# Performance work log

Measured on AMD Instinct MI355X. Metric: run time of the kernel, lower is better.

The kernel has to match this reference:

```python
import jax, jax.numpy as jnp
import numpy as np

B, DA, DU, W, MODES, L = 32, 2, 1, 64, 16, 8192


def setup_inputs() -> dict:
    key = jax.random.key(0)
    ks = jax.random.split(key, 9)
    x = jax.random.normal(ks[0], (B, DA, L), dtype=jnp.float32)
    P_w = jax.random.normal(ks[1], (W, DA), dtype=jnp.float32) * 0.1
    P_b = jax.random.normal(ks[2], (W,), dtype=jnp.float32) * 0.1
    # 4 spectral blocks: complex weights stored as real/imag parts [4, modes, out, in]
    scale = 1.0 / (W * W)
    k_wr = jax.random.uniform(ks[3], (4, MODES, W, W), dtype=jnp.float32) * scale
    k_wi = jax.random.uniform(ks[4], (4, MODES, W, W), dtype=jnp.float32) * scale
    conv_w = jax.random.normal(ks[5], (4, W, W), dtype=jnp.float32) * 0.1
    conv_b = jax.random.normal(ks[6], (4, W), dtype=jnp.float32) * 0.1
    Q_w = jax.random.normal(ks[7], (DU, W), dtype=jnp.float32) * 0.1
    Q_b = jax.random.normal(ks[8], (DU,), dtype=jnp.float32) * 0.1
    return {"x": x, "P_w": P_w, "P_b": P_b, "k_wr": k_wr, "k_wi": k_wi,
            "conv_w": conv_w, "conv_b": conv_b, "Q_w": Q_w, "Q_b": Q_b}


def _spectral(h, wr, wi):
    # h: [B, C, L]; wr/wi: [modes, O, I]
    hf = jnp.fft.rfft(h, axis=-1)                      # [B, C, F] complex
    w = wr + 1j * wi
    out_m = jnp.einsum('koi,bik->bok', w, hf[:, :, :MODES])  # [B, O, modes]
    F = hf.shape[-1]
    pad = jnp.zeros((h.shape[0], w.shape[1], F - MODES), dtype=out_m.dtype)
    full = jnp.concatenate([out_m, pad], axis=-1)
    return jnp.fft.irfft(full, n=h.shape[-1], axis=-1)


def reference(x, P_w, P_b, k_wr, k_wi, conv_w, conv_b, Q_w, Q_b):
    # lifting 1x1 conv: [B, da, L] -> [B, W, L]
    h = jnp.einsum('oc,bcl->bol', P_w, x) + P_b[None, :, None]
    for i in range(4):
        x1 = _spectral(h, k_wr[i], k_wi[i])
        x2 = jnp.einsum('oc,bcl->bol', conv_w[i], h) + conv_b[i][None, :, None]
        h = jax.nn.gelu(x1 + x2, approximate=False)
    out = jnp.einsum('oc,bcl->bol', Q_w, h) + Q_b[None, :, None]
    return out
```

## Files before the change

kernel.cpp:

```cpp
#include <hip/hip_runtime.h>
#include <math.h>

#define B 32
#define DA 2
#define DU 1
#define W 64
#define MODES 16
#define L 8192
#define LMASK 8191
#define LT 128

typedef __attribute__((ext_vector_type(8))) short short8;
typedef __attribute__((ext_vector_type(4))) float floatx4;

#define N_H (B*W*L)
#define OFF_H 0
#define N_HF (B*W*MODES)
#define OFF_HFR (OFF_H + N_H)
#define OFF_HFI (OFF_HFR + N_HF)
#define N_GT (B*W*32)
#define OFF_GT  (OFF_HFI + N_HF)
#define OFF_BTH (OFF_GT + N_GT)
#define N_BTW (32*L/2)
#define OFF_BTL (OFF_BTH + N_BTW)
#define OFF_BFH (OFF_BTL + N_BTW)
#define N_BF (256*2*16*32/2)
#define OFF_BFL (OFF_BFH + N_BF)
#define OFF_CWH (OFF_BFL + N_BF)
#define OFF_CWL (OFF_CWH + 8192)
#define OFF_P2  (OFF_CWL + 8192)

__device__ __forceinline__ unsigned packsplit(float v) {
    unsigned u = __float_as_uint(v);
    unsigned hi = u & 0xffff0000u;
    float lo = v - __uint_as_float(hi);
    return hi | (__float_as_uint(lo) >> 16);
}
__device__ __forceinline__ void fsplit(float v, unsigned short& h, unsigned short& l) {
    unsigned u = __float_as_uint(v);
    h = (unsigned short)(u >> 16);
    float lof = v - __uint_as_float(u & 0xffff0000u);
    l = (unsigned short)(__float_as_uint(lof) >> 16);
}

__global__ void k_tables(short* __restrict__ BTh, short* __restrict__ BTl,
                         short* __restrict__ BFhi, short* __restrict__ BFlo,
                         const float* __restrict__ cw,
                         short* __restrict__ CWFh, short* __restrict__ CWFl) {
    if (blockIdx.x < 512) {
        int idx = blockIdx.x * 256 + threadIdx.x;
        if (idx >= MODES * L) return;
        int k = idx >> 13;
        int l = idx & LMASK;
        int m = (k * l) & LMASK;
        float ang = 6.28318530717958647692f * ((float)m / (float)L);
        float s, c;
        sincosf(ang, &s, &c);
        unsigned short hh, ll;
        fsplit(c, hh, ll);
        BTh[(size_t)l * 32 + k] = (short)hh;  BTl[(size_t)l * 32 + k] = (short)ll;
        int sstep = l >> 5, qj = l & 31;
        int idx_re = ((sstep * 2 + 0) * 16 + k) * 32 + qj;
        BFhi[idx_re] = (short)hh;  BFlo[idx_re] = (short)ll;
        fsplit(s, hh, ll);
        BTh[(size_t)l * 32 + 16 + k] = (short)hh;  BTl[(size_t)l * 32 + 16 + k] = (short)ll;
        unsigned short nh, nl;
        fsplit(-s, nh, nl);
        int idx_im = ((sstep * 2 + 1) * 16 + k) * 32 + qj;
        BFhi[idx_im] = (short)nh;  BFlo[idx_im] = (short)nl;
    } else {
        int idx = (blockIdx.x - 512) * 256 + threadIdx.x;
        if (idx >= 4 * W * W) return;
        int layer = idx >> 12;
        int r = idx & 4095;
        int o = r >> 6, c = r & 63;
        int ot = o >> 4, n = o & 15, Kc = c >> 5, rest = c & 31;
        unsigned short hh, ll;
        fsplit(cw[idx], hh, ll);
        int di = layer * 4096 + ((ot * 2 + Kc) * 16 + n) * 32 + rest;
        CWFh[di] = (short)hh;  CWFl[di] = (short)ll;
    }
}

__device__ __forceinline__ void dft_partial(const unsigned* HsL,
                                            const short* __restrict__ BFhi,
                                            const short* __restrict__ BFlo,
                                            float* __restrict__ part2,
                                            int b, int l0, int t) {
    int wv = t >> 6, lane = t & 63, quad = lane >> 4, n = lane & 15;
    int sbase = l0 >> 5;
    const unsigned* arow = HsL + (wv * 16 + n) * 132 + quad * 8;
    floatx4 accR = {0.f, 0.f, 0.f, 0.f}, accI = {0.f, 0.f, 0.f, 0.f};
#pragma unroll
    for (int ks = 0; ks < 4; ks++) {
        const uint4* ap = (const uint4*)(arow + ks * 32);
        uint4 a0 = ap[0], a1 = ap[1];
        unsigned av[8] = {a0.x, a0.y, a0.z, a0.w, a1.x, a1.y, a1.z, a1.w};
        union { short8 v; unsigned short u[8]; } ah, al;
#pragma unroll
        for (int j = 0; j < 8; j++) {
            ah.u[j] = (unsigned short)(av[j] >> 16);
            al.u[j] = (unsigned short)(av[j] & 0xffffu);
        }
        int s = sbase + ks;
        const short* bb = BFhi + ((size_t)(s * 2) * 16 + n) * 32 + quad * 8;
        const short* lb = BFlo + ((size_t)(s * 2) * 16 + n) * 32 + quad * 8;
        short8 BhR = *(const short8*)bb;
        short8 BlR = *(const short8*)lb;
        short8 BhI = *(const short8*)(bb + 512);
        short8 BlI = *(const short8*)(lb + 512);
        accR = __builtin_amdgcn_mfma_f32_16x16x32_bf16(ah.v, BhR, accR, 0, 0, 0);
        accR = __builtin_amdgcn_mfma_f32_16x16x32_bf16(ah.v, BlR, accR, 0, 0, 0);
        accR = __builtin_amdgcn_mfma_f32_16x16x32_bf16(al.v, BhR, accR, 0, 0, 0);
        accI = __builtin_amdgcn_mfma_f32_16x16x32_bf16(ah.v, BhI, accI, 0, 0, 0);
        accI = __builtin_amdgcn_mfma_f32_16x16x32_bf16(ah.v, BlI, accI, 0, 0, 0);
        accI = __builtin_amdgcn_mfma_f32_16x16x32_bf16(al.v, BhI, accI, 0, 0, 0);
    }
    float* pr = part2 + (size_t)(l0 >> 7) * 65536
                      + ((size_t)b * 64 + wv * 16 + quad * 4) * 32 + n;
#pragma unroll
    for (int r = 0; r < 4; r++) {
        pr[(size_t)r * 32]      = accR[r];
        pr[(size_t)r * 32 + 16] = accI[r];
    }
}

__global__ __launch_bounds__(256) void k_lift(const float* __restrict__ x,
                                              const float* __restrict__ Pw,
                                              const float* __restrict__ Pb,
                                              unsigned* __restrict__ h,
                                              const short* __restrict__ BFhi,
                                              const short* __restrict__ BFlo,
                                              float* __restrict__ part2) {
    __shared__ unsigned HsL[64 * 132];
    int t = threadIdx.x;
    int b = blockIdx.y;
    int l0 = blockIdx.x * LT;
    int lq = t & 31, c8 = t >> 5;
    float4 x0 = *((const float4*)(x + (size_t)(b * 2 + 0) * L + l0) + lq);
    float4 x1 = *((const float4*)(x + (size_t)(b * 2 + 1) * L + l0) + lq);
#pragma unroll
    for (int cc = 0; cc < 8; cc++) {
        int c = c8 * 8 + cc;
        float w0 = Pw[c * 2 + 0], w1 = Pw[c * 2 + 1], pb = Pb[c];
        uint4 pv;
        pv.x = packsplit(fmaf(w0, x0.x, fmaf(w1, x1.x, pb)));
        pv.y = packsplit(fmaf(w0, x0.y, fmaf(w1, x1.y, pb)));
        pv.z = packsplit(fmaf(w0, x0.z, fmaf(w1, x1.z, pb)));
        pv.w = packsplit(fmaf(w0, x0.w, fmaf(w1, x1.w, pb)));
        *(uint4*)(h + ((size_t)b * W + c) * L + l0 + lq * 4) = pv;
        *(uint4*)&HsL[c * 132 + lq * 4] = pv;
    }
    __syncthreads();
    dft_partial(HsL, BFhi, BFlo, part2, b, l0, t);
}

__global__ void k_red(const float* __restrict__ part2, float* __restrict__ hf) {
    int idx = blockIdx.x * 256 + threadIdx.x;
    float s = 0.f;
#pragma unroll 16
    for (int c = 0; c < 64; c++) s += part2[(size_t)c * 65536 + idx];
    int row = idx >> 5, kp = idx & 31;
    if (kp < 16) hf[row * 16 + kp] = s;
    else         hf[32768 + row * 16 + (kp - 16)] = s;
}

__global__ __launch_bounds__(256) void k_mix(const float* __restrict__ hfr,
                                             const float* __restrict__ hfi,
                                             const float* __restrict__ kwr,
                                             const float* __restrict__ kwi,
                                             unsigned* __restrict__ Gt) {
    __shared__ float wrT[64 * 65], wiT[64 * 65];
    int t = threadIdx.x;
    int k = blockIdx.x;
    const float* wr = kwr + k * 4096;
    const float* wi = kwi + k * 4096;
    for (int i = t; i < 4096; i += 256) {
        int o = i >> 6, c = i & 63;
        wrT[c * 65 + o] = wr[i];
        wiT[c * 65 + o] = wi[i];
    }
    __syncthreads();
    int o = t & 63, bq = t >> 6;
    int b = blockIdx.y * 4 + bq;
    float accr = 0.f, acci = 0.f;
#pragma unroll 8
    for (int c = 0; c < W; c++) {
        float hr = hfr[(b * 64 + c) * 16 + k];
        float hi = hfi[(b * 64 + c) * 16 + k];
        float wrv = wrT[c * 65 + o], wiv = wiT[c * 65 + o];
        accr = fmaf(wrv, hr, fmaf(-wiv, hi, accr));
        acci = fmaf(wrv, hi, fmaf(wiv, hr, acci));
    }
    float sc = (k == 0) ? (1.f / (float)L) : (2.f / (float)L);
    float gi = (k == 0) ? 0.f : -acci * sc;
    Gt[((size_t)b * 64 + o) * 32 + k]      = packsplit(accr * sc);
    Gt[((size_t)b * 64 + o) * 32 + 16 + k] = packsplit(gi);
}

__device__ __forceinline__ float erf_fast(float x) {
    float ax = fabsf(x);
    float tinv = __builtin_amdgcn_rcpf(fmaf(0.3275911f, ax, 1.f));
    float p = fmaf(1.061405429f, tinv, -1.453152027f);
    p = fmaf(p, tinv, 1.421413741f);
    p = fmaf(p, tinv, -0.284496736f);
    p = fmaf(p, tinv, 0.254829592f);
    p = p * tinv;
    float e = fmaf(-p, __expf(-ax * ax), 1.f);
    return copysignf(e, x);
}

__global__ __launch_bounds__(256, 4) void k_combine(
    unsigned* __restrict__ h, const short* __restrict__ BTh, const short* __restrict__ BTl,
    const unsigned* __restrict__ Gt,
    const short* __restrict__ cwfh, const short* __restrict__ cwfl,
    const float* __restrict__ cb,
    const short* __restrict__ BFhi, const short* __restrict__ BFlo,
    float* __restrict__ part2, int emit,
    const float* __restrict__ Qw, const float* __restrict__ Qb,
    float* __restrict__ outbuf, int proj) {
    __shared__ unsigned Hs[64 * 132];
    int t = threadIdx.x;
    int b = blockIdx.y;
    int l0 = blockIdx.x * LT;

    int lane = t & 63, wv = t >> 6;
    int quad = lane >> 4, n = lane & 15;

    unsigned rawB[2][2][8];
    short8 Th[2], Tl[2];
#pragma unroll
    for (int lt = 0; lt < 2; lt++) {
        int lg = l0 + wv * 32 + lt * 16 + n;
        const unsigned* hb = h + (size_t)b * W * L + lg;
#pragma unroll
        for (int Kc = 0; Kc < 2; Kc++) {
#pragma unroll
            for (int j = 0; j < 8; j++) {
                int c = Kc * 32 + quad * 8 + j;
                rawB[lt][Kc][j] = hb[(size_t)c * L];
            }
        }
        Th[lt] = *(const short8*)(BTh + (size_t)lg * 32 + quad * 8);
        Tl[lt] = *(const short8*)(BTl + (size_t)lg * 32 + quad * 8);
    }
    short8 Bh[2][2], Bl[2][2];
#pragma unroll
    for (int lt = 0; lt < 2; lt++) {
#pragma unroll
        for (int Kc = 0; Kc < 2; Kc++) {
            union { short8 v; unsigned short u[8]; } uh, ul;
#pragma unroll
            for (int j = 0; j < 8; j++) {
                unsigned x = rawB[lt][Kc][j];
                uh.u[j] = (unsigned short)(x >> 16);
                ul.u[j] = (unsigned short)(x & 0xffffu);
            }
            Bh[lt][Kc] = uh.v; Bl[lt][Kc] = ul.v;
        }
    }

    float pacc[2] = {0.f, 0.f};

#pragma unroll 2
    for (int ot = 0; ot < 4; ot++) {
        int oa = ot * 16 + n;
        short8 Wh[2], Wl[2];
#pragma unroll
        for (int Kc = 0; Kc < 2; Kc++) {
            int wi = ((ot * 2 + Kc) * 16 + n) * 32 + quad * 8;
            Wh[Kc] = *(const short8*)(cwfh + wi);
            Wl[Kc] = *(const short8*)(cwfl + wi);
        }
        short8 Gh, Gl;
        {
            const uint4* gp = (const uint4*)(Gt + ((size_t)b * W + oa) * 32 + quad * 8);
            uint4 g0 = gp[0], g1 = gp[1];
            unsigned gv[8] = {g0.x, g0.y, g0.z, g0.w, g1.x, g1.y, g1.z, g1.w};
            union { short8 v; unsigned short u[8]; } ah, al;
#pragma unroll
            for (int j = 0; j < 8; j++) {
                ah.u[j] = (unsigned short)(gv[j] >> 16);
                al.u[j] = (unsigned short)(gv[j] & 0xffffu);
            }
            Gh = ah.v; Gl = al.v;
        }

#pragma unroll
        for (int lt = 0; lt < 2; lt++) {
            floatx4 acc = {0.f, 0.f, 0.f, 0.f};
#pragma unroll
            for (int Kc = 0; Kc < 2; Kc++) {
                acc = __builtin_amdgcn_mfma_f32_16x16x32_bf16(Wh[Kc], Bh[lt][Kc], acc, 0, 0, 0);
                acc = __builtin_amdgcn_mfma_f32_16x16x32_bf16(Wh[Kc], Bl[lt][Kc], acc, 0, 0, 0);
                acc = __builtin_amdgcn_mfma_f32_16x16x32_bf16(Wl[Kc], Bh[lt][Kc], acc, 0, 0, 0);
            }
            acc = __builtin_amdgcn_mfma_f32_16x16x32_bf16(Gh, Th[lt], acc, 0, 0, 0);
            acc = __builtin_amdgcn_mfma_f32_16x16x32_bf16(Gh, Tl[lt], acc, 0, 0, 0);
            acc = __builtin_amdgcn_mfma_f32_16x16x32_bf16(Gl, Th[lt], acc, 0, 0, 0);
            int lloc = wv * 32 + lt * 16 + n;
            int lg = l0 + lloc;
#pragma unroll
            for (int r = 0; r < 4; r++) {
                int od = ot * 16 + quad * 4 + r;
                float v = acc[r] + cb[od];
                float g = 0.5f * v * (1.f + erf_fast(v * 0.70710678118654752440f));
                if (proj) {
                    pacc[lt] = fmaf(Qw[od], g, pacc[lt]);
                } else {
                    unsigned p = packsplit(g);
                    h[((size_t)b * W + od) * L + lg] = p;
                    if (emit) Hs[od * 132 + lloc] = p;
                }
            }
        }
    }
    if (emit) {
        __syncthreads();
        dft_partial(Hs, BFhi, BFlo, part2, b, l0, t);
    }
    if (proj) {
        float qb = Qb[0];
#pragma unroll
        for (int lt = 0; lt < 2; lt++) {
            float v = pacc[lt];
            v += __shfl_xor(v, 16, 64);
            v += __shfl_xor(v, 32, 64);
            if (quad == 0)
                outbuf[(size_t)b * L + l0 + wv * 32 + lt * 16 + n] = v + qb;
        }
    }
}

extern "C" void kernel_launch(void* const* d_in, const int* in_sizes, int n_in,
                              void* d_out, int out_size, void* d_ws, size_t ws_size,
                              hipStream_t stream) {
    const float* x   = (const float*)d_in[0];
    const float* Pw  = (const float*)d_in[1];
    const float* Pb  = (const float*)d_in[2];
    const float* kwr = (const float*)d_in[3];
    const float* kwi = (const float*)d_in[4];
    const float* cw  = (const float*)d_in[5];
    const float* cb  = (const float*)d_in[6];
    const float* Qw  = (const float*)d_in[7];
    const float* Qb  = (const float*)d_in[8];

    float* ws = (float*)d_ws;
    unsigned* h    = (unsigned*)(ws + OFF_H);
    float*    hfr  = ws + OFF_HFR;
    float*    hfi  = ws + OFF_HFI;
    unsigned* Gt   = (unsigned*)(ws + OFF_GT);
    short*    BTh  = (short*)(ws + OFF_BTH);
    short*    BTl  = (short*)(ws + OFF_BTL);
    short*    BFhi = (short*)(ws + OFF_BFH);
    short*    BFlo = (short*)(ws + OFF_BFL);
    short*    CWFh = (short*)(ws + OFF_CWH);
    short*    CWFl = (short*)(ws + OFF_CWL);
    float*    part2 = ws + OFF_P2;

    k_tables<<<512 + 64, 256, 0, stream>>>(BTh, BTl, BFhi, BFlo, cw, CWFh, CWFl);
    k_lift<<<dim3(L / LT, B), 256, 0, stream>>>(x, Pw, Pb, h, BFhi, BFlo, part2);

    for (int i = 0; i < 4; i++) {
        k_red<<<65536 / 256, 256, 0, stream>>>(part2, hfr);
        k_mix<<<dim3(MODES, B / 4), 256, 0, stream>>>(hfr, hfi,
                                                      kwr + (size_t)i * MODES * W * W,
                                                      kwi + (size_t)i * MODES * W * W,
                                                      Gt);
        k_combine<<<dim3(L / LT, B), 256, 0, stream>>>(h, BTh, BTl, Gt,
                                                       CWFh + (size_t)i * 4096,
                                                       CWFl + (size_t)i * 4096,
                                                       cb + (size_t)i * W,
                                                       BFhi, BFlo, part2,
                                                       (i < 3) ? 1 : 0,
                                                       Qw, Qb, (float*)d_out,
                                                       (i == 3) ? 1 : 0);
    }
}
```

Before: 298.7 us.

## Replace partial-sum buffer and reduction kernel with atomic accumulation into double-buffered spectra

The DFT partials were written to a large per-tile buffer and summed by a separate k_red kernel. They are now accumulated directly into a spectrum buffer with float atomics. Two spectrum buffers alternate, with the next one zeroed inside k_mix and the first zeroed in k_tables. This removes one kernel launch per layer and a large partial-buffer write/read. The shared-memory tile also drops its padding in favour of an XOR swizzle, and launch bounds rise to 5 blocks per CU. The costs are atomic contention on 64K addresses and nondeterministic summation order.

```diff
diff --git a/kernel.cpp b/kernel.cpp
--- a/kernel.cpp
+++ b/kernel.cpp
@@ -16,10 +16,10 @@
 #define N_H (B*W*L)
 #define OFF_H 0
 #define N_HF (B*W*MODES)
-#define OFF_HFR (OFF_H + N_H)
-#define OFF_HFI (OFF_HFR + N_HF)
+#define OFF_HF0 (OFF_H + N_H)
+#define OFF_HF1 (OFF_HF0 + 2*N_HF)
 #define N_GT (B*W*32)
-#define OFF_GT  (OFF_HFI + N_HF)
+#define OFF_GT  (OFF_HF1 + 2*N_HF)
 #define OFF_BTH (OFF_GT + N_GT)
 #define N_BTW (32*L/2)
 #define OFF_BTL (OFF_BTH + N_BTW)
@@ -28,7 +28,6 @@
 #define OFF_BFL (OFF_BFH + N_BF)
 #define OFF_CWH (OFF_BFL + N_BF)
 #define OFF_CWL (OFF_CWH + 8192)
-#define OFF_P2  (OFF_CWL + 8192)
 
 __device__ __forceinline__ unsigned packsplit(float v) {
     unsigned u = __float_as_uint(v);
@@ -46,7 +45,8 @@
 __global__ void k_tables(short* __restrict__ BTh, short* __restrict__ BTl,
                          short* __restrict__ BFhi, short* __restrict__ BFlo,
                          const float* __restrict__ cw,
-                         short* __restrict__ CWFh, short* __restrict__ CWFl) {
+                         short* __restrict__ CWFh, short* __restrict__ CWFl,
+                         float* __restrict__ hf0) {
     if (blockIdx.x < 512) {
         int idx = blockIdx.x * 256 + threadIdx.x;
         if (idx >= MODES * L) return;
@@ -68,7 +68,7 @@
         fsplit(-s, nh, nl);
         int idx_im = ((sstep * 2 + 1) * 16 + k) * 32 + qj;
         BFhi[idx_im] = (short)nh;  BFlo[idx_im] = (short)nl;
-    } else {
+    } else if (blockIdx.x < 576) {
         int idx = (blockIdx.x - 512) * 256 + threadIdx.x;
         if (idx >= 4 * W * W) return;
         int layer = idx >> 12;
@@ -79,22 +79,29 @@
         fsplit(cw[idx], hh, ll);
         int di = layer * 4096 + ((ot * 2 + Kc) * 16 + n) * 32 + rest;
         CWFh[di] = (short)hh;  CWFl[di] = (short)ll;
+    } else {
+        int idx = (blockIdx.x - 576) * 256 + threadIdx.x;
+        float4 z = {0.f, 0.f, 0.f, 0.f};
+        *(float4*)(hf0 + (size_t)idx * 4) = z;
     }
 }
 
 __device__ __forceinline__ void dft_partial(const unsigned* HsL,
                                             const short* __restrict__ BFhi,
                                             const short* __restrict__ BFlo,
-                                            float* __restrict__ part2,
+                                            float* __restrict__ hfacc,
                                             int b, int l0, int t) {
     int wv = t >> 6, lane = t & 63, quad = lane >> 4, n = lane & 15;
     int sbase = l0 >> 5;
-    const unsigned* arow = HsL + (wv * 16 + n) * 132 + quad * 8;
+    int c = wv * 16 + n;
+    int swz = (c & 7) << 2;
+    const unsigned* arow = HsL + c * 128;
     floatx4 accR = {0.f, 0.f, 0.f, 0.f}, accI = {0.f, 0.f, 0.f, 0.f};
 #pragma unroll
     for (int ks = 0; ks < 4; ks++) {
-        const uint4* ap = (const uint4*)(arow + ks * 32);
-        uint4 a0 = ap[0], a1 = ap[1];
+        int col = quad * 8 + ks * 32;
+        uint4 a0 = *(const uint4*)(arow + (col ^ swz));
+        uint4 a1 = *(const uint4*)(arow + ((col + 4) ^ swz));
         unsigned av[8] = {a0.x, a0.y, a0.z, a0.w, a1.x, a1.y, a1.z, a1.w};
         union { short8 v; unsigned short u[8]; } ah, al;
 #pragma unroll
@@ -116,23 +123,22 @@
         accI = __builtin_amdgcn_mfma_f32_16x16x32_bf16(ah.v, BlI, accI, 0, 0, 0);
         accI = __builtin_amdgcn_mfma_f32_16x16x32_bf16(al.v, BhI, accI, 0, 0, 0);
     }
-    float* pr = part2 + (size_t)(l0 >> 7) * 65536
-                      + ((size_t)b * 64 + wv * 16 + quad * 4) * 32 + n;
+    float* pr = hfacc + ((size_t)(b * 64 + wv * 16 + quad * 4)) * 16 + n;
 #pragma unroll
     for (int r = 0; r < 4; r++) {
-        pr[(size_t)r * 32]      = accR[r];
-        pr[(size_t)r * 32 + 16] = accI[r];
-    }
-}
-
-__global__ __launch_bounds__(256) void k_lift(const float* __restrict__ x,
-                                              const float* __restrict__ Pw,
-                                              const float* __restrict__ Pb,
-                                              unsigned* __restrict__ h,
-                                              const short* __restrict__ BFhi,
-                                              const short* __restrict__ BFlo,
-                                              float* __restrict__ part2) {
-    __shared__ unsigned HsL[64 * 132];
+        unsafeAtomicAdd(pr + (size_t)r * 16, accR[r]);
+        unsafeAtomicAdd(pr + (size_t)r * 16 + 32768, accI[r]);
+    }
+}
+
+__global__ __launch_bounds__(256, 5) void k_lift(const float* __restrict__ x,
+                                                 const float* __restrict__ Pw,
+                                                 const float* __restrict__ Pb,
+                                                 unsigned* __restrict__ h,
+                                                 const short* __restrict__ BFhi,
+                                                 const short* __restrict__ BFlo,
+                                                 float* __restrict__ hfacc) {
+    __shared__ unsigned HsL[64 * 128];
     int t = threadIdx.x;
     int b = blockIdx.y;
     int l0 = blockIdx.x * LT;
@@ -149,30 +155,26 @@
         pv.z = packsplit(fmaf(w0, x0.z, fmaf(w1, x1.z, pb)));
         pv.w = packsplit(fmaf(w0, x0.w, fmaf(w1, x1.w, pb)));
         *(uint4*)(h + ((size_t)b * W + c) * L + l0 + lq * 4) = pv;
-        *(uint4*)&HsL[c * 132 + lq * 4] = pv;
+        *(uint4*)&HsL[c * 128 + ((lq * 4) ^ ((c & 7) << 2))] = pv;
     }
     __syncthreads();
-    dft_partial(HsL, BFhi, BFlo, part2, b, l0, t);
-}
-
-__global__ void k_red(const float* __restrict__ part2, float* __restrict__ hf) {
-    int idx = blockIdx.x * 256 + threadIdx.x;
-    float s = 0.f;
-#pragma unroll 16
-    for (int c = 0; c < 64; c++) s += part2[(size_t)c * 65536 + idx];
-    int row = idx >> 5, kp = idx & 31;
-    if (kp < 16) hf[row * 16 + kp] = s;
-    else         hf[32768 + row * 16 + (kp - 16)] = s;
+    dft_partial(HsL, BFhi, BFlo, hfacc, b, l0, t);
 }
 
 __global__ __launch_bounds__(256) void k_mix(const float* __restrict__ hfr,
                                              const float* __restrict__ hfi,
                                              const float* __restrict__ kwr,
                                              const float* __restrict__ kwi,
-                                             unsigned* __restrict__ Gt) {
+                                             unsigned* __restrict__ Gt,
+                                             float* __restrict__ hfz) {
     __shared__ float wrT[64 * 65], wiT[64 * 65];
     int t = threadIdx.x;
     int k = blockIdx.x;
+    {
+        int fid = (blockIdx.y * 16 + blockIdx.x) * 256 + t;
+        float2 z = {0.f, 0.f};
+        *(float2*)(hfz + (size_t)fid * 2) = z;
+    }
     const float* wr = kwr + k * 4096;
     const float* wi = kwi + k * 4096;
     for (int i = t; i < 4096; i += 256) {
@@ -210,16 +212,16 @@
     return copysignf(e, x);
 }
 
-__global__ __launch_bounds__(256, 4) void k_combine(
+__global__ __launch_bounds__(256, 5) void k_combine(
     unsigned* __restrict__ h, const short* __restrict__ BTh, const short* __restrict__ BTl,
     const unsigned* __restrict__ Gt,
     const short* __restrict__ cwfh, const short* __restrict__ cwfl,
     const float* __restrict__ cb,
     const short* __restrict__ BFhi, const short* __restrict__ BFlo,
-    float* __restrict__ part2, int emit,
+    float* __restrict__ hfacc, int emit,
     const float* __restrict__ Qw, const float* __restrict__ Qb,
     float* __restrict__ outbuf, int proj) {
-    __shared__ unsigned Hs[64 * 132];
+    __shared__ unsigned Hs[64 * 128];
     int t = threadIdx.x;
     int b = blockIdx.y;
     int l0 = blockIdx.x * LT;
@@ -310,14 +312,14 @@
                 } else {
                     unsigned p = packsplit(g);
                     h[((size_t)b * W + od) * L + lg] = p;
-                    if (emit) Hs[od * 132 + lloc] = p;
+                    if (emit) Hs[od * 128 + (lloc ^ ((od & 7) << 2))] = p;
                 }
             }
         }
     }
     if (emit) {
         __syncthreads();
-        dft_partial(Hs, BFhi, BFlo, part2, b, l0, t);
+        dft_partial(Hs, BFhi, BFlo, hfacc, b, l0, t);
     }
     if (proj) {
         float qb = Qb[0];
@@ -347,8 +349,8 @@
 
     float* ws = (float*)d_ws;
     unsigned* h    = (unsigned*)(ws + OFF_H);
-    float*    hfr  = ws + OFF_HFR;
-    float*    hfi  = ws + OFF_HFI;
+    float*    hf0  = ws + OFF_HF0;
+    float*    hf1  = ws + OFF_HF1;
     unsigned* Gt   = (unsigned*)(ws + OFF_GT);
     short*    BTh  = (short*)(ws + OFF_BTH);
     short*    BTl  = (short*)(ws + OFF_BTL);
@@ -356,22 +358,23 @@
     short*    BFlo = (short*)(ws + OFF_BFL);
     short*    CWFh = (short*)(ws + OFF_CWH);
     short*    CWFl = (short*)(ws + OFF_CWL);
-    float*    part2 = ws + OFF_P2;
-
-    k_tables<<<512 + 64, 256, 0, stream>>>(BTh, BTl, BFhi, BFlo, cw, CWFh, CWFl);
-    k_lift<<<dim3(L / LT, B), 256, 0, stream>>>(x, Pw, Pb, h, BFhi, BFlo, part2);
+    float*    hfbuf[2] = {hf0, hf1};
+
+    k_tables<<<640, 256, 0, stream>>>(BTh, BTl, BFhi, BFlo, cw, CWFh, CWFl, hf0);
+    k_lift<<<dim3(L / LT, B), 256, 0, stream>>>(x, Pw, Pb, h, BFhi, BFlo, hf0);
 
     for (int i = 0; i < 4; i++) {
-        k_red<<<65536 / 256, 256, 0, stream>>>(part2, hfr);
-        k_mix<<<dim3(MODES, B / 4), 256, 0, stream>>>(hfr, hfi,
+        float* hcur = hfbuf[i & 1];
+        float* hnxt = hfbuf[(i + 1) & 1];
+        k_mix<<<dim3(MODES, B / 4), 256, 0, stream>>>(hcur, hcur + 2 * N_HF / 2,
                                                       kwr + (size_t)i * MODES * W * W,
                                                       kwi + (size_t)i * MODES * W * W,
-                                                      Gt);
+                                                      Gt, hnxt);
         k_combine<<<dim3(L / LT, B), 256, 0, stream>>>(h, BTh, BTl, Gt,
                                                        CWFh + (size_t)i * 4096,
                                                        CWFl + (size_t)i * 4096,
                                                        cb + (size_t)i * W,
-                                                       BFhi, BFlo, part2,
+                                                       BFhi, BFlo, hnxt,
                                                        (i < 3) ? 1 : 0,
                                                        Qw, Qb, (float*)d_out,
                                                        (i == 3) ? 1 : 0);
```

After: 443.3 us. +48.4%, slower.
